# Kernel tuning notes

Measured on AMD Instinct MI355X. Metric: run time of the kernel, lower is better.

Reference implementation:

```python
import jax, jax.numpy as jnp
import numpy as np


def setup_inputs() -> dict:
    key = jax.random.key(0)
    kq, kk, kv = jax.random.split(key, 3)
    B, H, T, D = 2, 8, 8192, 64
    return {
        "Q": jax.random.normal(kq, (B, H, T, D), dtype=jnp.float32),
        "K": jax.random.normal(kk, (B, H, T, D), dtype=jnp.float32),
        "V": jax.random.normal(kv, (B, H, T, D), dtype=jnp.float32),
        "window_size": 512,
    }


def _gather_bands(x, nb, Wn):
    # x: [B,H,T,D] -> [B,H,nb,3*Wn,D], key blocks (i-1, i, i+1) per query block i
    B, H, T, D = x.shape
    xb = x.reshape(B, H, nb, Wn, D)
    xp = jnp.pad(xb, ((0, 0), (0, 0), (1, 1), (0, 0), (0, 0)))
    return jnp.concatenate([xp[:, :, i:i + nb] for i in range(3)], axis=3)


def reference(Q, K, V, window_size):
    # Sliding-window attention: softmax over keys with |q_idx - kv_idx| <= window_size,
    # computed block-sparsely (only the 3 neighboring key blocks per query block).
    B, H, T, D = Q.shape
    Wn = int(window_size)
    assert T % Wn == 0
    nb = T // Wn
    scale = 1.0 / (D ** 0.5)

    Qb = Q.reshape(B, H, nb, Wn, D)
    Kw = _gather_bands(K, nb, Wn)  # [B,H,nb,3W,D]
    Vw = _gather_bands(V, nb, Wn)

    # scores within the band: [B,H,nb,W,3W]
    s = jnp.einsum('bhnqd,bhnkd->bhnqk', Qb, Kw) * scale

    # exact band mask: global q = n*W + q_loc, global kv = (n-1)*W + k_loc
    q_loc = jnp.arange(Wn)[:, None]
    k_loc = jnp.arange(3 * Wn)[None, :]
    band = jnp.abs(q_loc + Wn - k_loc) <= Wn          # [W, 3W]
    kv_g = (jnp.arange(nb)[:, None] - 1) * Wn + jnp.arange(3 * Wn)[None, :]  # [nb, 3W]
    valid = (kv_g >= 0) & (kv_g < T)
    mask = band[None, :, :] & valid[:, None, :]        # [nb, W, 3W]

    s = jnp.where(mask[None, None], s, -jnp.inf)
    p = jax.nn.softmax(s, axis=-1)
    o = jnp.einsum('bhnqk,bhnkd->bhnqd', p, Vw)
    return o.reshape(B, H, T, D)
```

## Files before the change

### kernel.cpp

```cpp
#include <hip/hip_runtime.h>
#include <hip/hip_bf16.h>
#include <stdint.h>

typedef __attribute__((ext_vector_type(8))) short bf16x8;
typedef __attribute__((ext_vector_type(4))) short bf16x4;
typedef __attribute__((ext_vector_type(4))) float f32x4;

#define T_SEQ   8192
#define D_HEAD  64
#define NHEADS  16
#define WIN     512
#define BQ      128
#define BK      64
#define NTILES  (T_SEQ / BK)
#define LDSR    72
#define MASKVAL (-1.0e6f)

#define WS_NEEDED ((size_t)2 * NHEADS * T_SEQ * D_HEAD * 2)

#define MFMA16(a,b,c) __builtin_amdgcn_mfma_f32_16x16x16bf16_1k(a,b,c,0,0,0)

extern "C" __device__ __attribute__((const)) float __ocml_native_exp2_f32(float);
__device__ __forceinline__ float fexp2(float x) { return __ocml_native_exp2_f32(x); }

#define GLDS16(g, l) __builtin_amdgcn_global_load_lds( \
    (const __attribute__((address_space(1))) void*)(g), \
    (__attribute__((address_space(3))) void*)(l), 16, 0, 0)

__device__ __forceinline__ short f2bf(float f) {
    union { float f; uint32_t u; } v; v.f = f;
    return (short)((v.u + 0x7FFFu + ((v.u >> 16) & 1u)) >> 16);
}

__device__ __forceinline__ uint32_t pkbf2(float lo, float hi) {
    union { __hip_bfloat162 h; uint32_t u; } c;
    c.h = __float22bfloat162_rn(make_float2(lo, hi));
    return c.u;
}

__global__ __launch_bounds__(256, 2)
void prep_kv(const float* __restrict__ Kg, const float* __restrict__ Vg,
             short* __restrict__ Kb, short* __restrict__ Vt)
{
    __shared__ float vt[64 * 65];
    const int tid  = threadIdx.x;
    const int tile = blockIdx.x & (NTILES - 1);
    const int head = blockIdx.x >> 7;
    const size_t off = ((size_t)head * T_SEQ + (size_t)tile * BK) * D_HEAD;

    const float* ks = Kg + off;
    short* kd = Kb + off;
    #pragma unroll
    for (int i = 0; i < 2; ++i) {
        int L = tid + 256 * i;
        int row = L >> 3, c = L & 7;
        const float* s = ks + row * 64 + c * 8;
        float4 a = *(const float4*)s;
        float4 b = *(const float4*)(s + 4);
        short out[8] = { f2bf(a.x), f2bf(a.y), f2bf(a.z), f2bf(a.w),
                         f2bf(b.x), f2bf(b.y), f2bf(b.z), f2bf(b.w) };
        *(bf16x8*)(kd + (row * 8 + (c ^ (row & 7))) * 8) = *(bf16x8*)out;
    }

    const float* vs = Vg + off;
    #pragma unroll
    for (int i = 0; i < 4; ++i) {
        int idx = tid + 256 * i;
        int row = idx >> 4, c4 = (idx & 15) << 2;
        float4 v = *(const float4*)(vs + row * D_HEAD + c4);
        *(float4*)&vt[row * 65 + c4] = v;
    }
    __syncthreads();
    short* vd = Vt + ((size_t)head * NTILES + tile) * (BK * D_HEAD);
    {
        int d = tid >> 2, kq = (tid & 3) << 4;
        int c = kq >> 3;
        short out[16];
        #pragma unroll
        for (int j = 0; j < 16; ++j) out[j] = f2bf(vt[(kq + j) * 65 + d]);
        *(bf16x8*)(vd + (d * 8 + ( c      ^ (d & 7))) * 8) = *(bf16x8*)&out[0];
        *(bf16x8*)(vd + (d * 8 + ((c + 1) ^ (d & 7))) * 8) = *(bf16x8*)&out[8];
    }
}

__global__ __launch_bounds__(256, 4)
void swa_fwd(const float* __restrict__ Qg, const short* __restrict__ Kb,
             const short* __restrict__ Vt, float* __restrict__ Og)
{
    __shared__ short Ks[2][BK * D_HEAD];
    __shared__ short Vs[2][BK * D_HEAD];

    const int tid  = threadIdx.x;
    const int wave = tid >> 6;
    const int lane = tid & 63;
    const int lcol = lane & 15;
    const int quad = lane >> 4;
    const int rx   = lcol & 7;

    const int g    = blockIdx.x;
    const int head = g >> 6;
    const int qt   = ((g & 7) << 3) | ((g >> 3) & 7);
    const int q0   = qt * BQ;
    const int tq   = q0 >> 6;

    const float* Qp = Qg + (size_t)head * T_SEQ * D_HEAD;
    const short* Kp = Kb + (size_t)head * T_SEQ * D_HEAD;
    float*       Op = Og + (size_t)head * T_SEQ * D_HEAD;

    const float qscale = 0.125f * 1.44269504088896340736f;
    const int qrow_w = q0 + wave * 32;

    bf16x8 qf[2][2];
    #pragma unroll
    for (int mt = 0; mt < 2; ++mt) {
        const float* qptr = Qp + (size_t)(qrow_w + mt*16 + lcol) * D_HEAD + quad * 8;
        #pragma unroll
        for (int ks = 0; ks < 2; ++ks) {
            float4 a = *(const float4*)(qptr + ks*32);
            float4 b = *(const float4*)(qptr + ks*32 + 4);
            bf16x8 f;
            f[0]=f2bf(a.x*qscale); f[1]=f2bf(a.y*qscale); f[2]=f2bf(a.z*qscale); f[3]=f2bf(a.w*qscale);
            f[4]=f2bf(b.x*qscale); f[5]=f2bf(b.y*qscale); f[6]=f2bf(b.z*qscale); f[7]=f2bf(b.w*qscale);
            qf[mt][ks] = f;
        }
    }

    f32x4 oacc[2][4];
    float l_run[2];
    const f32x4 zero4 = {0.f, 0.f, 0.f, 0.f};
    #pragma unroll
    for (int mt = 0; mt < 2; ++mt) {
        l_run[mt] = 0.f;
        #pragma unroll
        for (int nt = 0; nt < 4; ++nt) oacc[mt][nt] = zero4;
    }

    int t0 = (q0 - WIN) >> 6;            if (t0 < 0) t0 = 0;
    int t1 = (q0 + BQ - 1 + WIN) >> 6;   if (t1 > NTILES - 1) t1 = NTILES - 1;

    const int ch0 = wave * 2, ch1 = wave * 2 + 1;

    {
        const short* ksrc = Kp + (size_t)t0 * (BK * D_HEAD);
        const short* vsrc = Vt + ((size_t)head * NTILES + t0) * (BK * D_HEAD);
        GLDS16(ksrc + ch0*512 + lane*8, &Ks[0][ch0*512]);
        GLDS16(ksrc + ch1*512 + lane*8, &Ks[0][ch1*512]);
        GLDS16(vsrc + ch0*512 + lane*8, &Vs[0][ch0*512]);
        GLDS16(vsrc + ch1*512 + lane*8, &Vs[0][ch1*512]);
    }
    asm volatile("s_waitcnt vmcnt(0)" ::: "memory");
    __syncthreads();

    int p = 0;
    for (int t = t0; t <= t1; ++t) {
        {
            const int tn = (t + 1 <= t1) ? t + 1 : t1;
            const short* ksrc = Kp + (size_t)tn * (BK * D_HEAD);
            const short* vsrc = Vt + ((size_t)head * NTILES + tn) * (BK * D_HEAD);
            short* kds = &Ks[p^1][0];
            short* vds = &Vs[p^1][0];
            GLDS16(ksrc + ch0*512 + lane*8, kds + ch0*512);
            GLDS16(ksrc + ch1*512 + lane*8, kds + ch1*512);
            GLDS16(vsrc + ch0*512 + lane*8, vds + ch0*512);
            GLDS16(vsrc + ch1*512 + lane*8, vds + ch1*512);
        }

        const short* Kcur = &Ks[p][0];
        const short* Vcur = &Vs[p][0];
        const bool edge = (t < tq - 6) || (t > tq + 7);

        #pragma unroll
        for (int h = 0; h < 2; ++h) {
            f32x4 sc[2][2];
            #pragma unroll
            for (int j = 0; j < 2; ++j) { sc[j][0] = zero4; sc[j][1] = zero4; }
            #pragma unroll
            for (int ks = 0; ks < 2; ++ks) {
                #pragma unroll
                for (int j = 0; j < 2; ++j) {
                    bf16x8 kf = *(const bf16x8*)&Kcur[((2*h+j)*16 + lcol)*64
                                                      + (((ks*4 + quad) ^ rx) << 3)];
                    sc[j][0] = __builtin_amdgcn_mfma_f32_16x16x32_bf16(kf, qf[0][ks], sc[j][0], 0,0,0);
                    sc[j][1] = __builtin_amdgcn_mfma_f32_16x16x32_bf16(kf, qf[1][ks], sc[j][1], 0,0,0);
                }
            }

            if (edge) {
                #pragma unroll
                for (int j = 0; j < 2; ++j) {
                    const int kg0 = t*BK + (2*h+j)*16 + quad*4;
                    #pragma unroll
                    for (int mt = 0; mt < 2; ++mt) {
                        const int qg = qrow_w + mt*16 + lcol;
                        #pragma unroll
                        for (int r = 0; r < 4; ++r) {
                            int dq = qg - (kg0 + r);
                            if (dq > WIN || dq < -WIN) sc[j][mt][r] = MASKVAL;
                        }
                    }
                }
            }

            #pragma unroll
            for (int j = 0; j < 2; ++j) {
                const int kt = 2*h + j;
                bf16x4 vf[4];
                #pragma unroll
                for (int nt = 0; nt < 4; ++nt)
                    vf[nt] = *(const bf16x4*)&Vcur[(nt*16 + lcol)*64
                                                   + (((kt*2 + (quad>>1)) ^ rx) << 3)
                                                   + ((quad & 1) << 2)];
                #pragma unroll
                for (int mt = 0; mt < 2; ++mt) {
                    float p0 = fexp2(sc[j][mt][0]);
                    float p1 = fexp2(sc[j][mt][1]);
                    float p2 = fexp2(sc[j][mt][2]);
                    float p3 = fexp2(sc[j][mt][3]);
                    l_run[mt] += (p0 + p1) + (p2 + p3);
                    union { int2 i; bf16x4 v; } pf;
                    pf.i = make_int2((int)pkbf2(p0, p1), (int)pkbf2(p2, p3));
                    #pragma unroll
                    for (int nt = 0; nt < 4; ++nt)
                        oacc[mt][nt] = MFMA16(vf[nt], pf.v, oacc[mt][nt]);
                }
            }
        }

        asm volatile("s_waitcnt vmcnt(0)" ::: "memory");
        __syncthreads();
        p ^= 1;
    }

    #pragma unroll
    for (int mt = 0; mt < 2; ++mt) {
        float l = l_run[mt];
        l += __shfl_xor(l, 16, 64);
        l += __shfl_xor(l, 32, 64);
        float inv = 1.0f / l;
        const int qg = qrow_w + mt*16 + lcol;
        float* op = Op + (size_t)qg * D_HEAD + quad*4;
        #pragma unroll
        for (int nt = 0; nt < 4; ++nt) {
            float4 o = { oacc[mt][nt][0]*inv, oacc[mt][nt][1]*inv,
                         oacc[mt][nt][2]*inv, oacc[mt][nt][3]*inv };
            *(float4*)(op + nt*16) = o;
        }
    }
}

#define BQF     128
__global__ __launch_bounds__(256, 4)
void swa_fused_fb(const float* __restrict__ Qg, const float* __restrict__ Kg,
                  const float* __restrict__ Vg, float* __restrict__ Og)
{
    __shared__ short Ksf[BK * LDSR];
    __shared__ short Vsf[D_HEAD * LDSR];
    __shared__ float Vtmp[BK * 65];

    const int tid  = threadIdx.x;
    const int wave = tid >> 6;
    const int lane = tid & 63;
    const int lcol = lane & 15;
    const int quad = lane >> 4;

    const int g    = blockIdx.x;
    const int head = g >> 6;
    const int qt   = ((g & 7) << 3) | ((g >> 3) & 7);
    const int q0   = qt * BQF;
    const int tq   = q0 >> 6;

    const size_t hoff = (size_t)head * T_SEQ * D_HEAD;
    const float* Qp = Qg + hoff;
    const float* Kp = Kg + hoff;
    const float* Vp = Vg + hoff;
    float*       Op = Og + hoff;

    const float qscale = 0.125f * 1.44269504088896340736f;
    const int qrow_w = q0 + wave * 32;

    bf16x8 qf[2][2];
    #pragma unroll
    for (int mt = 0; mt < 2; ++mt) {
        const float* qptr = Qp + (size_t)(qrow_w + mt*16 + lcol) * D_HEAD + quad * 8;
        #pragma unroll
        for (int ks = 0; ks < 2; ++ks) {
            float4 a = *(const float4*)(qptr + ks*32);
            float4 b = *(const float4*)(qptr + ks*32 + 4);
            bf16x8 f;
            f[0]=f2bf(a.x*qscale); f[1]=f2bf(a.y*qscale); f[2]=f2bf(a.z*qscale); f[3]=f2bf(a.w*qscale);
            f[4]=f2bf(b.x*qscale); f[5]=f2bf(b.y*qscale); f[6]=f2bf(b.z*qscale); f[7]=f2bf(b.w*qscale);
            qf[mt][ks] = f;
        }
    }

    f32x4 oacc[2][4];
    float l_run[2];
    const f32x4 zero4 = {0.f, 0.f, 0.f, 0.f};
    #pragma unroll
    for (int mt = 0; mt < 2; ++mt) {
        l_run[mt] = 0.f;
        #pragma unroll
        for (int nt = 0; nt < 4; ++nt) oacc[mt][nt] = zero4;
    }

    int t0 = (q0 - WIN) >> 6;            if (t0 < 0) t0 = 0;
    int t1 = (q0 + BQF - 1 + WIN) >> 6;  if (t1 > NTILES - 1) t1 = NTILES - 1;

    const int krow0 = tid >> 3, kc = (tid & 7) << 3;
    const int krow1 = krow0 + 32;
    const int vrow  = tid >> 4, vc = (tid & 15) << 2;
    const int td    = tid >> 2, tkq = (tid & 3) << 4;

    for (int t = t0; t <= t1; ++t) {
        const float* ksrc = Kp + (size_t)t * BK * D_HEAD;
        const float* vsrc = Vp + (size_t)t * BK * D_HEAD;
        float4 k00 = *(const float4*)(ksrc + krow0*D_HEAD + kc);
        float4 k01 = *(const float4*)(ksrc + krow0*D_HEAD + kc + 4);
        float4 k10 = *(const float4*)(ksrc + krow1*D_HEAD + kc);
        float4 k11 = *(const float4*)(ksrc + krow1*D_HEAD + kc + 4);
        float4 v0  = *(const float4*)(vsrc + (vrow     )*D_HEAD + vc);
        float4 v1  = *(const float4*)(vsrc + (vrow + 16)*D_HEAD + vc);
        float4 v2  = *(const float4*)(vsrc + (vrow + 32)*D_HEAD + vc);
        float4 v3  = *(const float4*)(vsrc + (vrow + 48)*D_HEAD + vc);

        __syncthreads();

        *(float4*)&Vtmp[(vrow     )*65 + vc] = v0;
        *(float4*)&Vtmp[(vrow + 16)*65 + vc] = v1;
        *(float4*)&Vtmp[(vrow + 32)*65 + vc] = v2;
        *(float4*)&Vtmp[(vrow + 48)*65 + vc] = v3;
        *(int4*)&Ksf[krow0*LDSR + kc] = make_int4((int)pkbf2(k00.x,k00.y), (int)pkbf2(k00.z,k00.w),
                                                  (int)pkbf2(k01.x,k01.y), (int)pkbf2(k01.z,k01.w));
        *(int4*)&Ksf[krow1*LDSR + kc] = make_int4((int)pkbf2(k10.x,k10.y), (int)pkbf2(k10.z,k10.w),
                                                  (int)pkbf2(k11.x,k11.y), (int)pkbf2(k11.z,k11.w));

        __syncthreads();

        {
            uint32_t w0 = pkbf2(Vtmp[(tkq+ 0)*65 + td], Vtmp[(tkq+ 1)*65 + td]);
            uint32_t w1 = pkbf2(Vtmp[(tkq+ 2)*65 + td], Vtmp[(tkq+ 3)*65 + td]);
            uint32_t w2 = pkbf2(Vtmp[(tkq+ 4)*65 + td], Vtmp[(tkq+ 5)*65 + td]);
            uint32_t w3 = pkbf2(Vtmp[(tkq+ 6)*65 + td], Vtmp[(tkq+ 7)*65 + td]);
            uint32_t w4 = pkbf2(Vtmp[(tkq+ 8)*65 + td], Vtmp[(tkq+ 9)*65 + td]);
            uint32_t w5 = pkbf2(Vtmp[(tkq+10)*65 + td], Vtmp[(tkq+11)*65 + td]);
            uint32_t w6 = pkbf2(Vtmp[(tkq+12)*65 + td], Vtmp[(tkq+13)*65 + td]);
            uint32_t w7 = pkbf2(Vtmp[(tkq+14)*65 + td], Vtmp[(tkq+15)*65 + td]);
            *(int4*)&Vsf[td*LDSR + tkq]     = make_int4((int)w0,(int)w1,(int)w2,(int)w3);
            *(int4*)&Vsf[td*LDSR + tkq + 8] = make_int4((int)w4,(int)w5,(int)w6,(int)w7);
        }

        __syncthreads();

        const bool edge = (t < tq - 6) || (t > tq + 7);

        #pragma unroll
        for (int h = 0; h < 2; ++h) {
            f32x4 sc[2][2];
            #pragma unroll
            for (int j = 0; j < 2; ++j) { sc[j][0] = zero4; sc[j][1] = zero4; }
            #pragma unroll
            for (int ks = 0; ks < 2; ++ks) {
                #pragma unroll
                for (int j = 0; j < 2; ++j) {
                    bf16x8 kf = *(const bf16x8*)&Ksf[((2*h+j)*16 + lcol)*LDSR + ks*32 + quad*8];
                    sc[j][0] = __builtin_amdgcn_mfma_f32_16x16x32_bf16(kf, qf[0][ks], sc[j][0], 0,0,0);
                    sc[j][1] = __builtin_amdgcn_mfma_f32_16x16x32_bf16(kf, qf[1][ks], sc[j][1], 0,0,0);
                }
            }

            if (edge) {
                #pragma unroll
                for (int j = 0; j < 2; ++j) {
                    const int kg0 = t*BK + (2*h+j)*16 + quad*4;
                    #pragma unroll
                    for (int mt = 0; mt < 2; ++mt) {
                        const int qg = qrow_w + mt*16 + lcol;
                        #pragma unroll
                        for (int r = 0; r < 4; ++r) {
                            int dq = qg - (kg0 + r);
                            if (dq > WIN || dq < -WIN) sc[j][mt][r] = MASKVAL;
                        }
                    }
                }
            }

            #pragma unroll
            for (int j = 0; j < 2; ++j) {
                const int kt = 2*h + j;
                bf16x4 vf[4];
                #pragma unroll
                for (int nt = 0; nt < 4; ++nt)
                    vf[nt] = *(const bf16x4*)&Vsf[(nt*16 + lcol)*LDSR + kt*16 + quad*4];
                #pragma unroll
                for (int mt = 0; mt < 2; ++mt) {
                    float p0 = fexp2(sc[j][mt][0]);
                    float p1 = fexp2(sc[j][mt][1]);
                    float p2 = fexp2(sc[j][mt][2]);
                    float p3 = fexp2(sc[j][mt][3]);
                    l_run[mt] += (p0 + p1) + (p2 + p3);
                    union { int2 i; bf16x4 v; } pf;
                    pf.i = make_int2((int)pkbf2(p0, p1), (int)pkbf2(p2, p3));
                    #pragma unroll
                    for (int nt = 0; nt < 4; ++nt)
                        oacc[mt][nt] = MFMA16(vf[nt], pf.v, oacc[mt][nt]);
                }
            }
        }
    }

    #pragma unroll
    for (int mt = 0; mt < 2; ++mt) {
        float l = l_run[mt];
        l += __shfl_xor(l, 16, 64);
        l += __shfl_xor(l, 32, 64);
        float inv = 1.0f / l;
        const int qg = qrow_w + mt*16 + lcol;
        float* op = Op + (size_t)qg * D_HEAD + quad*4;
        #pragma unroll
        for (int nt = 0; nt < 4; ++nt) {
            float4 o = { oacc[mt][nt][0]*inv, oacc[mt][nt][1]*inv,
                         oacc[mt][nt][2]*inv, oacc[mt][nt][3]*inv };
            *(float4*)(op + nt*16) = o;
        }
    }
}

extern "C" void kernel_launch(void* const* d_in, const int* in_sizes, int n_in,
                              void* d_out, int out_size, void* d_ws, size_t ws_size,
                              hipStream_t stream)
{
    const float* Q = (const float*)d_in[0];
    const float* K = (const float*)d_in[1];
    const float* V = (const float*)d_in[2];
    float* O = (float*)d_out;

    if (ws_size >= WS_NEEDED) {
        short* Kb = (short*)d_ws;
        short* Vt = Kb + (size_t)NHEADS * T_SEQ * D_HEAD;
        prep_kv<<<dim3(NHEADS * NTILES), dim3(256), 0, stream>>>(K, V, Kb, Vt);
        swa_fwd<<<dim3(NHEADS * (T_SEQ / BQ)), dim3(256), 0, stream>>>(Q, Kb, Vt, O);
    } else {
        swa_fused_fb<<<dim3(NHEADS * (T_SEQ / BQF)), dim3(256), 0, stream>>>(Q, K, V, O);
    }
}
```

Measured before the change: 185.5 us.

## Repack V tile for wide LDS reads, MFMA row-sum, unroll double-buffer loop

The V transpose prep kernel now interleaves key rows so each lane can load one 8-wide bf16 vector covering both j halves, replacing four 4-wide LDS reads per j. The softmax denominator is accumulated with an extra MFMA against a ones vector instead of scalar adds and the final cross-lane shuffles. The tile loop is unrolled by two via a lambda so buffer parity is a compile-time constant. The ones-MFMA sums bf16-rounded probabilities, which slightly changes normalisation precision and adds MFMA work.

```diff
diff --git a/kernel.cpp b/kernel.cpp
--- a/kernel.cpp
+++ b/kernel.cpp
@@ -73,13 +73,17 @@
     __syncthreads();
     short* vd = Vt + ((size_t)head * NTILES + tile) * (BK * D_HEAD);
     {
-        int d = tid >> 2, kq = (tid & 3) << 4;
-        int c = kq >> 3;
-        short out[16];
-        #pragma unroll
-        for (int j = 0; j < 16; ++j) out[j] = f2bf(vt[(kq + j) * 65 + d]);
-        *(bf16x8*)(vd + (d * 8 + ( c      ^ (d & 7))) * 8) = *(bf16x8*)&out[0];
-        *(bf16x8*)(vd + (d * 8 + ((c + 1) ^ (d & 7))) * 8) = *(bf16x8*)&out[8];
+        int d = tid >> 2, q = tid & 3;
+        #pragma unroll
+        for (int h = 0; h < 2; ++h) {
+            int c = h * 4 + q;
+            short out[8];
+            #pragma unroll
+            for (int j = 0; j < 4; ++j) out[j]     = f2bf(vt[(h*32      + q*4 + j) * 65 + d]);
+            #pragma unroll
+            for (int j = 0; j < 4; ++j) out[4 + j] = f2bf(vt[(h*32 + 16 + q*4 + j) * 65 + d]);
+            *(bf16x8*)(vd + (d * 8 + (c ^ (d & 7))) * 8) = *(bf16x8*)out;
+        }
     }
 }
 
@@ -126,11 +130,13 @@
     }
 
     f32x4 oacc[2][4];
-    float l_run[2];
+    f32x4 lacc[2];
     const f32x4 zero4 = {0.f, 0.f, 0.f, 0.f};
-    #pragma unroll
-    for (int mt = 0; mt < 2; ++mt) {
-        l_run[mt] = 0.f;
+    const short oneb = (short)0x3F80;
+    const bf16x4 ones4 = {oneb, oneb, oneb, oneb};
+    #pragma unroll
+    for (int mt = 0; mt < 2; ++mt) {
+        lacc[mt] = zero4;
         #pragma unroll
         for (int nt = 0; nt < 4; ++nt) oacc[mt][nt] = zero4;
     }
@@ -151,26 +157,30 @@
     asm volatile("s_waitcnt vmcnt(0)" ::: "memory");
     __syncthreads();
 
-    int p = 0;
-    for (int t = t0; t <= t1; ++t) {
+    auto body = [&](int t, int P) {
         {
             const int tn = (t + 1 <= t1) ? t + 1 : t1;
             const short* ksrc = Kp + (size_t)tn * (BK * D_HEAD);
             const short* vsrc = Vt + ((size_t)head * NTILES + tn) * (BK * D_HEAD);
-            short* kds = &Ks[p^1][0];
-            short* vds = &Vs[p^1][0];
+            short* kds = &Ks[P^1][0];
+            short* vds = &Vs[P^1][0];
             GLDS16(ksrc + ch0*512 + lane*8, kds + ch0*512);
             GLDS16(ksrc + ch1*512 + lane*8, kds + ch1*512);
             GLDS16(vsrc + ch0*512 + lane*8, vds + ch0*512);
             GLDS16(vsrc + ch1*512 + lane*8, vds + ch1*512);
         }
 
-        const short* Kcur = &Ks[p][0];
-        const short* Vcur = &Vs[p][0];
+        const short* Kcur = &Ks[P][0];
+        const short* Vcur = &Vs[P][0];
         const bool edge = (t < tq - 6) || (t > tq + 7);
 
         #pragma unroll
         for (int h = 0; h < 2; ++h) {
+            bf16x8 vv[4];
+            #pragma unroll
+            for (int nt = 0; nt < 4; ++nt)
+                vv[nt] = *(const bf16x8*)&Vcur[(nt*16 + lcol)*64 + (((h*4 + quad) ^ rx) << 3)];
+
             f32x4 sc[2][2];
             #pragma unroll
             for (int j = 0; j < 2; ++j) { sc[j][0] = zero4; sc[j][1] = zero4; }
@@ -203,13 +213,194 @@
 
             #pragma unroll
             for (int j = 0; j < 2; ++j) {
+                bf16x4 vh[4];
+                #pragma unroll
+                for (int nt = 0; nt < 4; ++nt) {
+                    bf16x8 v8 = vv[nt];
+                    bf16x4 x = { v8[j*4+0], v8[j*4+1], v8[j*4+2], v8[j*4+3] };
+                    vh[nt] = x;
+                }
+                #pragma unroll
+                for (int mt = 0; mt < 2; ++mt) {
+                    float p0 = fexp2(sc[j][mt][0]);
+                    float p1 = fexp2(sc[j][mt][1]);
+                    float p2 = fexp2(sc[j][mt][2]);
+                    float p3 = fexp2(sc[j][mt][3]);
+                    union { int2 i; bf16x4 v; } pf;
+                    pf.i = make_int2((int)pkbf2(p0, p1), (int)pkbf2(p2, p3));
+                    lacc[mt] = MFMA16(ones4, pf.v, lacc[mt]);
+                    #pragma unroll
+                    for (int nt = 0; nt < 4; ++nt)
+                        oacc[mt][nt] = MFMA16(vh[nt], pf.v, oacc[mt][nt]);
+                }
+            }
+        }
+
+        asm volatile("s_waitcnt vmcnt(0)" ::: "memory");
+        __syncthreads();
+    };
+
+    int t = t0;
+    for (; t + 1 <= t1; t += 2) { body(t, 0); body(t + 1, 1); }
+    if (t <= t1) body(t, 0);
+
+    #pragma unroll
+    for (int mt = 0; mt < 2; ++mt) {
+        float inv = 1.0f / lacc[mt][0];
+        const int qg = qrow_w + mt*16 + lcol;
+        float* op = Op + (size_t)qg * D_HEAD + quad*4;
+        #pragma unroll
+        for (int nt = 0; nt < 4; ++nt) {
+            float4 o = { oacc[mt][nt][0]*inv, oacc[mt][nt][1]*inv,
+                         oacc[mt][nt][2]*inv, oacc[mt][nt][3]*inv };
+            *(float4*)(op + nt*16) = o;
+        }
+    }
+}
+
+#define BQF     128
+__global__ __launch_bounds__(256, 4)
+void swa_fused_fb(const float* __restrict__ Qg, const float* __restrict__ Kg,
+                  const float* __restrict__ Vg, float* __restrict__ Og)
+{
+    __shared__ short Ksf[BK * LDSR];
+    __shared__ short Vsf[D_HEAD * LDSR];
+    __shared__ float Vtmp[BK * 65];
+
+    const int tid  = threadIdx.x;
+    const int wave = tid >> 6;
+    const int lane = tid & 63;
+    const int lcol = lane & 15;
+    const int quad = lane >> 4;
+
+    const int g    = blockIdx.x;
+    const int head = g >> 6;
+    const int qt   = ((g & 7) << 3) | ((g >> 3) & 7);
+    const int q0   = qt * BQF;
+    const int tq   = q0 >> 6;
+
+    const size_t hoff = (size_t)head * T_SEQ * D_HEAD;
+    const float* Qp = Qg + hoff;
+    const float* Kp = Kg + hoff;
+    const float* Vp = Vg + hoff;
+    float*       Op = Og + hoff;
+
+    const float qscale = 0.125f * 1.44269504088896340736f;
+    const int qrow_w = q0 + wave * 32;
+
+    bf16x8 qf[2][2];
+    #pragma unroll
+    for (int mt = 0; mt < 2; ++mt) {
+        const float* qptr = Qp + (size_t)(qrow_w + mt*16 + lcol) * D_HEAD + quad * 8;
+        #pragma unroll
+        for (int ks = 0; ks < 2; ++ks) {
+            float4 a = *(const float4*)(qptr + ks*32);
+            float4 b = *(const float4*)(qptr + ks*32 + 4);
+            bf16x8 f;
+            f[0]=f2bf(a.x*qscale); f[1]=f2bf(a.y*qscale); f[2]=f2bf(a.z*qscale); f[3]=f2bf(a.w*qscale);
+            f[4]=f2bf(b.x*qscale); f[5]=f2bf(b.y*qscale); f[6]=f2bf(b.z*qscale); f[7]=f2bf(b.w*qscale);
+            qf[mt][ks] = f;
+        }
+    }
+
+    f32x4 oacc[2][4];
+    float l_run[2];
+    const f32x4 zero4 = {0.f, 0.f, 0.f, 0.f};
+    #pragma unroll
+    for (int mt = 0; mt < 2; ++mt) {
+        l_run[mt] = 0.f;
+        #pragma unroll
+        for (int nt = 0; nt < 4; ++nt) oacc[mt][nt] = zero4;
+    }
+
+    int t0 = (q0 - WIN) >> 6;            if (t0 < 0) t0 = 0;
+    int t1 = (q0 + BQF - 1 + WIN) >> 6;  if (t1 > NTILES - 1) t1 = NTILES - 1;
+
+    const int krow0 = tid >> 3, kc = (tid & 7) << 3;
+    const int krow1 = krow0 + 32;
+    const int vrow  = tid >> 4, vc = (tid & 15) << 2;
+    const int td    = tid >> 2, tkq = (tid & 3) << 4;
+
+    for (int t = t0; t <= t1; ++t) {
+        const float* ksrc = Kp + (size_t)t * BK * D_HEAD;
+        const float* vsrc = Vp + (size_t)t * BK * D_HEAD;
+        float4 k00 = *(const float4*)(ksrc + krow0*D_HEAD + kc);
+        float4 k01 = *(const float4*)(ksrc + krow0*D_HEAD + kc + 4);
+        float4 k10 = *(const float4*)(ksrc + krow1*D_HEAD + kc);
+        float4 k11 = *(const float4*)(ksrc + krow1*D_HEAD + kc + 4);
+        float4 v0  = *(const float4*)(vsrc + (vrow     )*D_HEAD + vc);
+        float4 v1  = *(const float4*)(vsrc + (vrow + 16)*D_HEAD + vc);
+        float4 v2  = *(const float4*)(vsrc + (vrow + 32)*D_HEAD + vc);
+        float4 v3  = *(const float4*)(vsrc + (vrow + 48)*D_HEAD + vc);
+
+        __syncthreads();
+
+        *(float4*)&Vtmp[(vrow     )*65 + vc] = v0;
+        *(float4*)&Vtmp[(vrow + 16)*65 + vc] = v1;
+        *(float4*)&Vtmp[(vrow + 32)*65 + vc] = v2;
+        *(float4*)&Vtmp[(vrow + 48)*65 + vc] = v3;
+        *(int4*)&Ksf[krow0*LDSR + kc] = make_int4((int)pkbf2(k00.x,k00.y), (int)pkbf2(k00.z,k00.w),
+                                                  (int)pkbf2(k01.x,k01.y), (int)pkbf2(k01.z,k01.w));
+        *(int4*)&Ksf[krow1*LDSR + kc] = make_int4((int)pkbf2(k10.x,k10.y), (int)pkbf2(k10.z,k10.w),
+                                                  (int)pkbf2(k11.x,k11.y), (int)pkbf2(k11.z,k11.w));
+
+        __syncthreads();
+
+        {
+            uint32_t w0 = pkbf2(Vtmp[(tkq+ 0)*65 + td], Vtmp[(tkq+ 1)*65 + td]);
+            uint32_t w1 = pkbf2(Vtmp[(tkq+ 2)*65 + td], Vtmp[(tkq+ 3)*65 + td]);
+            uint32_t w2 = pkbf2(Vtmp[(tkq+ 4)*65 + td], Vtmp[(tkq+ 5)*65 + td]);
+            uint32_t w3 = pkbf2(Vtmp[(tkq+ 6)*65 + td], Vtmp[(tkq+ 7)*65 + td]);
+            uint32_t w4 = pkbf2(Vtmp[(tkq+ 8)*65 + td], Vtmp[(tkq+ 9)*65 + td]);
+            uint32_t w5 = pkbf2(Vtmp[(tkq+10)*65 + td], Vtmp[(tkq+11)*65 + td]);
+            uint32_t w6 = pkbf2(Vtmp[(tkq+12)*65 + td], Vtmp[(tkq+13)*65 + td]);
+            uint32_t w7 = pkbf2(Vtmp[(tkq+14)*65 + td], Vtmp[(tkq+15)*65 + td]);
+            *(int4*)&Vsf[td*LDSR + tkq]     = make_int4((int)w0,(int)w1,(int)w2,(int)w3);
+            *(int4*)&Vsf[td*LDSR + tkq + 8] = make_int4((int)w4,(int)w5,(int)w6,(int)w7);
+        }
+
+        __syncthreads();
+
+        const bool edge = (t < tq - 6) || (t > tq + 7);
+
+        #pragma unroll
+        for (int h = 0; h < 2; ++h) {
+            f32x4 sc[2][2];
+            #pragma unroll
+            for (int j = 0; j < 2; ++j) { sc[j][0] = zero4; sc[j][1] = zero4; }
+            #pragma unroll
+            for (int ks = 0; ks < 2; ++ks) {
+                #pragma unroll
+                for (int j = 0; j < 2; ++j) {
+                    bf16x8 kf = *(const bf16x8*)&Ksf[((2*h+j)*16 + lcol)*LDSR + ks*32 + quad*8];
+                    sc[j][0] = __builtin_amdgcn_mfma_f32_16x16x32_bf16(kf, qf[0][ks], sc[j][0], 0,0,0);
+                    sc[j][1] = __builtin_amdgcn_mfma_f32_16x16x32_bf16(kf, qf[1][ks], sc[j][1], 0,0,0);
+                }
+            }
+
+            if (edge) {
+                #pragma unroll
+                for (int j = 0; j < 2; ++j) {
+                    const int kg0 = t*BK + (2*h+j)*16 + quad*4;
+                    #pragma unroll
+                    for (int mt = 0; mt < 2; ++mt) {
+                        const int qg = qrow_w + mt*16 + lcol;
+                        #pragma unroll
+                        for (int r = 0; r < 4; ++r) {
+                            int dq = qg - (kg0 + r);
+                            if (dq > WIN || dq < -WIN) sc[j][mt][r] = MASKVAL;
+                        }
+                    }
+                }
+            }
+
+            #pragma unroll
+            for (int j = 0; j < 2; ++j) {
                 const int kt = 2*h + j;
                 bf16x4 vf[4];
                 #pragma unroll
                 for (int nt = 0; nt < 4; ++nt)
-                    vf[nt] = *(const bf16x4*)&Vcur[(nt*16 + lcol)*64
-                                                   + (((kt*2 + (quad>>1)) ^ rx) << 3)
-                                                   + ((quad & 1) << 2)];
+                    vf[nt] = *(const bf16x4*)&Vsf[(nt*16 + lcol)*LDSR + kt*16 + quad*4];
                 #pragma unroll
                 for (int mt = 0; mt < 2; ++mt) {
                     float p0 = fexp2(sc[j][mt][0]);
@@ -225,187 +416,6 @@
                 }
             }
         }
-
-        asm volatile("s_waitcnt vmcnt(0)" ::: "memory");
-        __syncthreads();
-        p ^= 1;
-    }
-
-    #pragma unroll
-    for (int mt = 0; mt < 2; ++mt) {
-        float l = l_run[mt];
-        l += __shfl_xor(l, 16, 64);
-        l += __shfl_xor(l, 32, 64);
-        float inv = 1.0f / l;
-        const int qg = qrow_w + mt*16 + lcol;
-        float* op = Op + (size_t)qg * D_HEAD + quad*4;
-        #pragma unroll
-        for (int nt = 0; nt < 4; ++nt) {
-            float4 o = { oacc[mt][nt][0]*inv, oacc[mt][nt][1]*inv,
-                         oacc[mt][nt][2]*inv, oacc[mt][nt][3]*inv };
-            *(float4*)(op + nt*16) = o;
-        }
-    }
-}
-
-#define BQF     128
-__global__ __launch_bounds__(256, 4)
-void swa_fused_fb(const float* __restrict__ Qg, const float* __restrict__ Kg,
-                  const float* __restrict__ Vg, float* __restrict__ Og)
-{
-    __shared__ short Ksf[BK * LDSR];
-    __shared__ short Vsf[D_HEAD * LDSR];
-    __shared__ float Vtmp[BK * 65];
-
-    const int tid  = threadIdx.x;
-    const int wave = tid >> 6;
-    const int lane = tid & 63;
-    const int lcol = lane & 15;
-    const int quad = lane >> 4;
-
-    const int g    = blockIdx.x;
-    const int head = g >> 6;
-    const int qt   = ((g & 7) << 3) | ((g >> 3) & 7);
-    const int q0   = qt * BQF;
-    const int tq   = q0 >> 6;
-
-    const size_t hoff = (size_t)head * T_SEQ * D_HEAD;
-    const float* Qp = Qg + hoff;
-    const float* Kp = Kg + hoff;
-    const float* Vp = Vg + hoff;
-    float*       Op = Og + hoff;
-
-    const float qscale = 0.125f * 1.44269504088896340736f;
-    const int qrow_w = q0 + wave * 32;
-
-    bf16x8 qf[2][2];
-    #pragma unroll
-    for (int mt = 0; mt < 2; ++mt) {
-        const float* qptr = Qp + (size_t)(qrow_w + mt*16 + lcol) * D_HEAD + quad * 8;
-        #pragma unroll
-        for (int ks = 0; ks < 2; ++ks) {
-            float4 a = *(const float4*)(qptr + ks*32);
-            float4 b = *(const float4*)(qptr + ks*32 + 4);
-            bf16x8 f;
-            f[0]=f2bf(a.x*qscale); f[1]=f2bf(a.y*qscale); f[2]=f2bf(a.z*qscale); f[3]=f2bf(a.w*qscale);
-            f[4]=f2bf(b.x*qscale); f[5]=f2bf(b.y*qscale); f[6]=f2bf(b.z*qscale); f[7]=f2bf(b.w*qscale);
-            qf[mt][ks] = f;
-        }
-    }
-
-    f32x4 oacc[2][4];
-    float l_run[2];
-    const f32x4 zero4 = {0.f, 0.f, 0.f, 0.f};
-    #pragma unroll
-    for (int mt = 0; mt < 2; ++mt) {
-        l_run[mt] = 0.f;
-        #pragma unroll
-        for (int nt = 0; nt < 4; ++nt) oacc[mt][nt] = zero4;
-    }
-
-    int t0 = (q0 - WIN) >> 6;            if (t0 < 0) t0 = 0;
-    int t1 = (q0 + BQF - 1 + WIN) >> 6;  if (t1 > NTILES - 1) t1 = NTILES - 1;
-
-    const int krow0 = tid >> 3, kc = (tid & 7) << 3;
-    const int krow1 = krow0 + 32;
-    const int vrow  = tid >> 4, vc = (tid & 15) << 2;
-    const int td    = tid >> 2, tkq = (tid & 3) << 4;
-
-    for (int t = t0; t <= t1; ++t) {
-        const float* ksrc = Kp + (size_t)t * BK * D_HEAD;
-        const float* vsrc = Vp + (size_t)t * BK * D_HEAD;
-        float4 k00 = *(const float4*)(ksrc + krow0*D_HEAD + kc);
-        float4 k01 = *(const float4*)(ksrc + krow0*D_HEAD + kc + 4);
-        float4 k10 = *(const float4*)(ksrc + krow1*D_HEAD + kc);
-        float4 k11 = *(const float4*)(ksrc + krow1*D_HEAD + kc + 4);
-        float4 v0  = *(const float4*)(vsrc + (vrow     )*D_HEAD + vc);
-        float4 v1  = *(const float4*)(vsrc + (vrow + 16)*D_HEAD + vc);
-        float4 v2  = *(const float4*)(vsrc + (vrow + 32)*D_HEAD + vc);
-        float4 v3  = *(const float4*)(vsrc + (vrow + 48)*D_HEAD + vc);
-
-        __syncthreads();
-
-        *(float4*)&Vtmp[(vrow     )*65 + vc] = v0;
-        *(float4*)&Vtmp[(vrow + 16)*65 + vc] = v1;
-        *(float4*)&Vtmp[(vrow + 32)*65 + vc] = v2;
-        *(float4*)&Vtmp[(vrow + 48)*65 + vc] = v3;
-        *(int4*)&Ksf[krow0*LDSR + kc] = make_int4((int)pkbf2(k00.x,k00.y), (int)pkbf2(k00.z,k00.w),
-                                                  (int)pkbf2(k01.x,k01.y), (int)pkbf2(k01.z,k01.w));
-        *(int4*)&Ksf[krow1*LDSR + kc] = make_int4((int)pkbf2(k10.x,k10.y), (int)pkbf2(k10.z,k10.w),
-                                                  (int)pkbf2(k11.x,k11.y), (int)pkbf2(k11.z,k11.w));
-
-        __syncthreads();
-
-        {
-            uint32_t w0 = pkbf2(Vtmp[(tkq+ 0)*65 + td], Vtmp[(tkq+ 1)*65 + td]);
-            uint32_t w1 = pkbf2(Vtmp[(tkq+ 2)*65 + td], Vtmp[(tkq+ 3)*65 + td]);
-            uint32_t w2 = pkbf2(Vtmp[(tkq+ 4)*65 + td], Vtmp[(tkq+ 5)*65 + td]);
-            uint32_t w3 = pkbf2(Vtmp[(tkq+ 6)*65 + td], Vtmp[(tkq+ 7)*65 + td]);
-            uint32_t w4 = pkbf2(Vtmp[(tkq+ 8)*65 + td], Vtmp[(tkq+ 9)*65 + td]);
-            uint32_t w5 = pkbf2(Vtmp[(tkq+10)*65 + td], Vtmp[(tkq+11)*65 + td]);
-            uint32_t w6 = pkbf2(Vtmp[(tkq+12)*65 + td], Vtmp[(tkq+13)*65 + td]);
-            uint32_t w7 = pkbf2(Vtmp[(tkq+14)*65 + td], Vtmp[(tkq+15)*65 + td]);
-            *(int4*)&Vsf[td*LDSR + tkq]     = make_int4((int)w0,(int)w1,(int)w2,(int)w3);
-            *(int4*)&Vsf[td*LDSR + tkq + 8] = make_int4((int)w4,(int)w5,(int)w6,(int)w7);
-        }
-
-        __syncthreads();
-
-        const bool edge = (t < tq - 6) || (t > tq + 7);
-
-        #pragma unroll
-        for (int h = 0; h < 2; ++h) {
-            f32x4 sc[2][2];
-            #pragma unroll
-            for (int j = 0; j < 2; ++j) { sc[j][0] = zero4; sc[j][1] = zero4; }
-            #pragma unroll
-            for (int ks = 0; ks < 2; ++ks) {
-                #pragma unroll
-                for (int j = 0; j < 2; ++j) {
-                    bf16x8 kf = *(const bf16x8*)&Ksf[((2*h+j)*16 + lcol)*LDSR + ks*32 + quad*8];
-                    sc[j][0] = __builtin_amdgcn_mfma_f32_16x16x32_bf16(kf, qf[0][ks], sc[j][0], 0,0,0);
-                    sc[j][1] = __builtin_amdgcn_mfma_f32_16x16x32_bf16(kf, qf[1][ks], sc[j][1], 0,0,0);
-                }
-            }
-
-            if (edge) {
-                #pragma unroll
-                for (int j = 0; j < 2; ++j) {
-                    const int kg0 = t*BK + (2*h+j)*16 + quad*4;
-                    #pragma unroll
-                    for (int mt = 0; mt < 2; ++mt) {
-                        const int qg = qrow_w + mt*16 + lcol;
-                        #pragma unroll
-                        for (int r = 0; r < 4; ++r) {
-                            int dq = qg - (kg0 + r);
-                            if (dq > WIN || dq < -WIN) sc[j][mt][r] = MASKVAL;
-                        }
-                    }
-                }
-            }
-
-            #pragma unroll
-            for (int j = 0; j < 2; ++j) {
-                const int kt = 2*h + j;
-                bf16x4 vf[4];
-                #pragma unroll
-                for (int nt = 0; nt < 4; ++nt)
-                    vf[nt] = *(const bf16x4*)&Vsf[(nt*16 + lcol)*LDSR + kt*16 + quad*4];
-                #pragma unroll
-                for (int mt = 0; mt < 2; ++mt) {
-                    float p0 = fexp2(sc[j][mt][0]);
-                    float p1 = fexp2(sc[j][mt][1]);
-                    float p2 = fexp2(sc[j][mt][2]);
-                    float p3 = fexp2(sc[j][mt][3]);
-                    l_run[mt] += (p0 + p1) + (p2 + p3);
-                    union { int2 i; bf16x4 v; } pf;
-                    pf.i = make_int2((int)pkbf2(p0, p1), (int)pkbf2(p2, p3));
-                    #pragma unroll
-                    for (int nt = 0; nt < 4; ++nt)
-                        oacc[mt][nt] = MFMA16(vf[nt], pf.v, oacc[mt][nt]);
-                }
-            }
-        }
     }
 
     #pragma unroll
```

New measurement: 186.8 us. About the same (+0.7%).
